# Kernel optimization log

Hardware: AMD Instinct MI355X
Metric: run time of the kernel (lower is better)

The kernel has to match this reference:

```python
import jax, jax.numpy as jnp
import numpy as np

B_SCALE = 1.3195079565048218
N_LEVELS = 16
BASE_RES = 16
MAX_PARAMS = 2 ** 19
N_POINTS = 1048576
PRIMES = (1, 2654435761, 805459861)  # uint32 hash primes (Instant-NGP)


def _level_meta():
    offsets, sizes, inds = [], [], []
    off = 0
    for i in range(N_LEVELS):
        res = int(np.ceil(BASE_RES * np.exp(i * np.log(B_SCALE)) - 1.0)) + 1
        p = res ** 3
        if p % 8 != 0:
            p = ((p + 7) // 8) * 8
        p = min(MAX_PARAMS, p)
        offsets.append(off)
        sizes.append(p)
        inds.append(res ** 3 <= p)  # dense (under_hash) vs hashed level
        off += p
    return offsets, sizes, inds, off


OFFSETS, SIZES, INDICATORS, TOTAL_PARAMS = _level_meta()
TOTAL_HASH_SIZE = TOTAL_PARAMS * 2  # == 11445040


def _encode_level(x01, table2, level):
    # x01: [N,3] in [0,1]; table2: [total_params, 2]
    scale = np.float32(BASE_RES * np.exp(level * np.log(B_SCALE)) - 1.0)
    resolution = np.uint32(np.ceil(scale) + 1)
    map_size = np.uint32(SIZES[level])
    pos = x01 * scale + 0.5
    grid_f = jnp.floor(pos)
    frac = pos - grid_f                           # [N,3] trilinear weights
    grid = grid_f.astype(jnp.uint32)              # [N,3]
    feat = jnp.zeros((x01.shape[0], 2), dtype=table2.dtype)
    primes = np.array(PRIMES, dtype=np.uint32)
    stride = np.array([1, int(resolution), int(resolution) * int(resolution)], dtype=np.uint32)
    for idx in range(8):  # 8 grid corners
        sel = np.array([(idx >> d) & 1 for d in range(3)], dtype=np.uint32)
        corner = grid + sel                       # [N,3] uint32
        w = jnp.prod(jnp.where(sel[None, :] == 1, frac, 1.0 - frac), axis=-1)  # [N]
        if INDICATORS[level]:
            c = corner * stride[None, :]
            h = c[:, 0] + c[:, 1] + c[:, 2]       # under_hash (dense indexing)
        else:
            c = corner * primes[None, :]          # uint32 wraparound multiply
            h = c[:, 0] ^ c[:, 1] ^ c[:, 2]       # fast_hash
        index = (h % map_size).astype(jnp.int32) + np.int32(OFFSETS[level])
        feat = feat + w[:, None] * table2[index]  # gather + trilinear blend
    return feat


def setup_inputs() -> dict:
    key = jax.random.key(0)
    k1, k2 = jax.random.split(key)
    positions = jax.random.uniform(k1, (N_POINTS, 3), dtype=jnp.float32, minval=-1.0, maxval=1.0)
    # random_initialize: (rand*2-1)*1e-4
    hash_table = jax.random.uniform(k2, (TOTAL_HASH_SIZE,), dtype=jnp.float32, minval=-1e-4, maxval=1e-4)
    return {"positions": positions, "hash_table": hash_table}


def reference(positions, hash_table):
    x01 = (positions + 1.0) * 0.5  # bound = 1
    table2 = hash_table.reshape(-1, 2)
    feats = [_encode_level(x01, table2, l) for l in range(N_LEVELS)]
    return jnp.concatenate(feats, axis=-1)  # [N, 32]
```

## Files before the change

kernel.cpp:

```cpp
#include <hip/hip_runtime.h>
#include <math.h>
#include <stdint.h>

#define NLV 16
#define NDENSE 6
#define NHASH 10

typedef float evf2 __attribute__((ext_vector_type(2)));

struct Params {
  float scale[NLV];
  uint32_t res[NLV];
  uint32_t msize[NLV];
  uint32_t offset[NLV];
};

struct ParamsD {
  float scale[NDENSE];
  uint32_t res[NDENSE];
  uint32_t msize[NDENSE];
  uint32_t offset[NDENSE];
};

__device__ __forceinline__ float ntload(const float* p) {
  return __builtin_nontemporal_load(p);
}

__global__ __launch_bounds__(256) void hash_level_kernel(
    const float* __restrict__ positions,
    const float* __restrict__ tbl,
    float2* __restrict__ tmp,
    float scale, uint32_t mask, int n)
{
  int t = blockIdx.x * 256 + threadIdx.x;
  int p0 = t * 2;
  if (p0 >= n) return;

  float xx[2], yy[2], zz[2];
  {
    evf2 a = __builtin_nontemporal_load(reinterpret_cast<const evf2*>(positions + 3*p0));
    evf2 b = __builtin_nontemporal_load(reinterpret_cast<const evf2*>(positions + 3*p0 + 2));
    evf2 c = __builtin_nontemporal_load(reinterpret_cast<const evf2*>(positions + 3*p0 + 4));
    xx[0] = a.x; yy[0] = a.y; zz[0] = b.x;
    xx[1] = b.y; yy[1] = c.x; zz[1] = c.y;
  }

  float r0[2], r1[2];
  #pragma unroll
  for (int q = 0; q < 2; ++q) {
    float x = (xx[q] + 1.0f) * 0.5f;
    float y = (yy[q] + 1.0f) * 0.5f;
    float z = (zz[q] + 1.0f) * 0.5f;

    float px = x * scale + 0.5f;
    float py = y * scale + 0.5f;
    float pz = z * scale + 0.5f;
    float fx = floorf(px), fy = floorf(py), fz = floorf(pz);
    float tx = px - fx, ty = py - fy, tz = pz - fz;
    uint32_t gx = (uint32_t)fx, gy = (uint32_t)fy, gz = (uint32_t)fz;

    float wxa = 1.0f - tx, wxb = tx;
    float wy_[2] = {1.0f - ty, ty};
    float wz_[2] = {1.0f - tz, tz};

    float f0 = 0.0f, f1 = 0.0f;

    if ((gx & 1u) == 0u) {
      #pragma unroll
      for (int cyz = 0; cyz < 4; ++cyz) {
        uint32_t cy = gy + (cyz & 1u);
        uint32_t cz = gz + (cyz >> 1);
        uint32_t hy = (cy * 2654435761u) ^ (cz * 805459861u);
        uint32_t ha = (gx ^ hy) & mask;
        float wyz = wy_[cyz & 1u] * wz_[cyz >> 1];
        float wa = wxa * wyz, wb = wxb * wyz;
        const float4 t4 = *reinterpret_cast<const float4*>(tbl + 2u * (ha & ~1u));
        float2 ta, tb;
        if (ha & 1u) { ta.x = t4.z; ta.y = t4.w; tb.x = t4.x; tb.y = t4.y; }
        else         { ta.x = t4.x; ta.y = t4.y; tb.x = t4.z; tb.y = t4.w; }
        f0 += wa * ta.x; f1 += wa * ta.y;
        f0 += wb * tb.x; f1 += wb * tb.y;
      }
    } else {
      #pragma unroll
      for (int cyz = 0; cyz < 4; ++cyz) {
        uint32_t cy = gy + (cyz & 1u);
        uint32_t cz = gz + (cyz >> 1);
        uint32_t hy = (cy * 2654435761u) ^ (cz * 805459861u);
        uint32_t ha = (gx ^ hy) & mask;
        uint32_t hb = ((gx + 1u) ^ hy) & mask;
        float wyz = wy_[cyz & 1u] * wz_[cyz >> 1];
        float wa = wxa * wyz, wb = wxb * wyz;
        const float2 ta = *reinterpret_cast<const float2*>(tbl + 2u * ha);
        const float2 tb = *reinterpret_cast<const float2*>(tbl + 2u * hb);
        f0 += wa * ta.x; f1 += wa * ta.y;
        f0 += wb * tb.x; f1 += wb * tb.y;
      }
    }
    r0[q] = f0; r1[q] = f1;
  }

  evf2 v0; v0.x = r0[0]; v0.y = r1[0];
  __builtin_nontemporal_store(v0, reinterpret_cast<evf2*>(tmp + p0));
  if (p0 + 1 < n) {
    evf2 v1; v1.x = r0[1]; v1.y = r1[1];
    __builtin_nontemporal_store(v1, reinterpret_cast<evf2*>(tmp + p0 + 1));
  }
}

__global__ __launch_bounds__(256) void dense_kernel(
    const float* __restrict__ positions,
    const float* __restrict__ table,
    float2* __restrict__ tmp,
    ParamsD prm, int n)
{
  int p = blockIdx.x * 256 + threadIdx.x;
  if (p >= n) return;

  float x = (ntload(positions + 3*p+0) + 1.0f) * 0.5f;
  float y = (ntload(positions + 3*p+1) + 1.0f) * 0.5f;
  float z = (ntload(positions + 3*p+2) + 1.0f) * 0.5f;

  #pragma unroll
  for (int l = 0; l < NDENSE; ++l) {
    const float s = prm.scale[l];
    const uint32_t res = prm.res[l];
    const uint32_t ms = prm.msize[l];
    const float* __restrict__ tbl = table + 2u * prm.offset[l];
    const uint32_t res2 = res * res;

    float px = x * s + 0.5f;
    float py = y * s + 0.5f;
    float pz = z * s + 0.5f;
    float fx = floorf(px), fy = floorf(py), fz = floorf(pz);
    float tx = px - fx, ty = py - fy, tz = pz - fz;
    uint32_t gx = (uint32_t)fx, gy = (uint32_t)fy, gz = (uint32_t)fz;

    float wxa = 1.0f - tx, wxb = tx;
    float wy_[2] = {1.0f - ty, ty};
    float wz_[2] = {1.0f - tz, tz};

    float f0 = 0.0f, f1 = 0.0f;
    #pragma unroll
    for (int cyz = 0; cyz < 4; ++cyz) {
      uint32_t cy = gy + (cyz & 1u);
      uint32_t cz = gz + ((cyz >> 1) & 1u);
      uint32_t h = gx + cy * res + cz * res2;
      if (h >= ms) h -= ms;
      float wyz = wy_[cyz & 1u] * wz_[(cyz >> 1) & 1u];
      float2 ta, tb;
      if (h + 1u < ms) {
        const float4 t4 = *reinterpret_cast<const float4*>(tbl + 2u * h);
        ta.x = t4.x; ta.y = t4.y; tb.x = t4.z; tb.y = t4.w;
      } else {
        ta = *reinterpret_cast<const float2*>(tbl + 2u * h);
        tb = *reinterpret_cast<const float2*>(tbl);
      }
      float wa = wxa * wyz, wb = wxb * wyz;
      f0 += wa * ta.x; f1 += wa * ta.y;
      f0 += wb * tb.x; f1 += wb * tb.y;
    }
    evf2 v; v.x = f0; v.y = f1;
    __builtin_nontemporal_store(v,
        reinterpret_cast<evf2*>(tmp + (size_t)(NHASH + l) * n + p));
  }
}

__global__ __launch_bounds__(256) void stream_pack_kernel(
    const float2* __restrict__ tmp,
    float* __restrict__ out, int n)
{
  int p = blockIdx.x * 256 + threadIdx.x;
  if (p >= n) return;

  evf2 dv[NDENSE];
  #pragma unroll
  for (int j = 0; j < NDENSE; ++j)
    dv[j] = __builtin_nontemporal_load(
        reinterpret_cast<const evf2*>(tmp + (size_t)(NHASH + j) * n + p));
  evf2 hv[NHASH];
  #pragma unroll
  for (int j = 0; j < NHASH; ++j)
    hv[j] = __builtin_nontemporal_load(
        reinterpret_cast<const evf2*>(tmp + (size_t)j * n + p));

  float4* o = reinterpret_cast<float4*>(out + (size_t)p * 32u);
  #pragma unroll
  for (int j = 0; j < 3; ++j)
    o[j] = make_float4(dv[2*j].x, dv[2*j].y, dv[2*j+1].x, dv[2*j+1].y);
  #pragma unroll
  for (int j = 0; j < 5; ++j)
    o[3 + j] = make_float4(hv[2*j].x, hv[2*j].y, hv[2*j+1].x, hv[2*j+1].y);
}

__global__ __launch_bounds__(256) void dense_pack_kernel(
    const float* __restrict__ positions,
    const float* __restrict__ table,
    const float2* __restrict__ tmp,
    float* __restrict__ out,
    ParamsD prm, int n)
{
  int p = blockIdx.x * 256 + threadIdx.x;
  if (p >= n) return;

  float x = (ntload(positions + 3*p+0) + 1.0f) * 0.5f;
  float y = (ntload(positions + 3*p+1) + 1.0f) * 0.5f;
  float z = (ntload(positions + 3*p+2) + 1.0f) * 0.5f;

  float acc[2*NDENSE];

  #pragma unroll
  for (int l = 0; l < NDENSE; ++l) {
    const float s = prm.scale[l];
    const uint32_t res = prm.res[l];
    const uint32_t ms = prm.msize[l];
    const float* __restrict__ tbl = table + 2u * prm.offset[l];
    const uint32_t res2 = res * res;

    float px = x * s + 0.5f;
    float py = y * s + 0.5f;
    float pz = z * s + 0.5f;
    float fx = floorf(px), fy = floorf(py), fz = floorf(pz);
    float tx = px - fx, ty = py - fy, tz = pz - fz;
    uint32_t gx = (uint32_t)fx, gy = (uint32_t)fy, gz = (uint32_t)fz;

    float wxa = 1.0f - tx, wxb = tx;
    float wy_[2] = {1.0f - ty, ty};
    float wz_[2] = {1.0f - tz, tz};

    float f0 = 0.0f, f1 = 0.0f;
    #pragma unroll
    for (int cyz = 0; cyz < 4; ++cyz) {
      uint32_t cy = gy + (cyz & 1u);
      uint32_t cz = gz + ((cyz >> 1) & 1u);
      uint32_t h = gx + cy * res + cz * res2;
      if (h >= ms) h -= ms;
      float wyz = wy_[cyz & 1u] * wz_[(cyz >> 1) & 1u];
      float2 ta, tb;
      if (h + 1u < ms) {
        const float4 t4 = *reinterpret_cast<const float4*>(tbl + 2u * h);
        ta.x = t4.x; ta.y = t4.y; tb.x = t4.z; tb.y = t4.w;
      } else {
        ta = *reinterpret_cast<const float2*>(tbl + 2u * h);
        tb = *reinterpret_cast<const float2*>(tbl);
      }
      float wa = wxa * wyz, wb = wxb * wyz;
      f0 += wa * ta.x; f1 += wa * ta.y;
      f0 += wb * tb.x; f1 += wb * tb.y;
    }
    acc[2*l]   = f0;
    acc[2*l+1] = f1;
  }

  evf2 hv[NHASH];
  #pragma unroll
  for (int j = 0; j < NHASH; ++j)
    hv[j] = __builtin_nontemporal_load(
        reinterpret_cast<const evf2*>(tmp + (size_t)j * n + p));

  float4* o = reinterpret_cast<float4*>(out + (size_t)p * 32u);
  o[0] = make_float4(acc[0], acc[1], acc[2],  acc[3]);
  o[1] = make_float4(acc[4], acc[5], acc[6],  acc[7]);
  o[2] = make_float4(acc[8], acc[9], acc[10], acc[11]);
  #pragma unroll
  for (int j = 0; j < 5; ++j)
    o[3 + j] = make_float4(hv[2*j].x, hv[2*j].y, hv[2*j+1].x, hv[2*j+1].y);
}

__global__ __launch_bounds__(256) void hash_enc_kernel(
    const float* __restrict__ positions,
    const float* __restrict__ table,
    float* __restrict__ out,
    Params prm, int n)
{
  int p = blockIdx.x * 256 + threadIdx.x;
  if (p >= n) return;

  float x = (positions[3*p+0] + 1.0f) * 0.5f;
  float y = (positions[3*p+1] + 1.0f) * 0.5f;
  float z = (positions[3*p+2] + 1.0f) * 0.5f;

  float acc[32];

  #pragma unroll
  for (int l = 0; l < NLV; ++l) {
    const float s = prm.scale[l];
    const uint32_t res = prm.res[l];
    const uint32_t ms = prm.msize[l];
    const uint32_t off = prm.offset[l];

    float px = x * s + 0.5f;
    float py = y * s + 0.5f;
    float pz = z * s + 0.5f;
    float fx = floorf(px), fy = floorf(py), fz = floorf(pz);
    float tx = px - fx, ty = py - fy, tz = pz - fz;
    uint32_t gx = (uint32_t)fx, gy = (uint32_t)fy, gz = (uint32_t)fz;

    float wx[2] = {1.0f - tx, tx};
    float wy[2] = {1.0f - ty, ty};
    float wz[2] = {1.0f - tz, tz};

    float f0 = 0.0f, f1 = 0.0f;
    #pragma unroll
    for (int c = 0; c < 8; ++c) {
      uint32_t cx = gx + (c & 1u);
      uint32_t cy = gy + ((c >> 1) & 1u);
      uint32_t cz = gz + ((c >> 2) & 1u);
      uint32_t h;
      if (l < NDENSE) {
        h = cx + cy * res + cz * res * res;
        if (h >= ms) h -= ms;
      } else {
        h = cx ^ (cy * 2654435761u) ^ (cz * 805459861u);
        h &= (ms - 1u);
      }
      float w = (wx[c & 1u] * wy[(c >> 1) & 1u]) * wz[(c >> 2) & 1u];
      const float2 t = *reinterpret_cast<const float2*>(table + 2u * (h + off));
      f0 += w * t.x;
      f1 += w * t.y;
    }
    acc[2*l]   = f0;
    acc[2*l+1] = f1;
  }

  float4* o = reinterpret_cast<float4*>(out + (size_t)p * 32u);
  #pragma unroll
  for (int k = 0; k < 8; ++k)
    o[k] = make_float4(acc[4*k+0], acc[4*k+1], acc[4*k+2], acc[4*k+3]);
}

extern "C" void kernel_launch(void* const* d_in, const int* in_sizes, int n_in,
                              void* d_out, int out_size, void* d_ws, size_t ws_size,
                              hipStream_t stream) {
  const float* positions = (const float*)d_in[0];
  const float* table     = (const float*)d_in[1];
  float* out             = (float*)d_out;
  int n = in_sizes[0] / 3;

  Params prm;
  const double lnb = log(1.3195079565048218);
  uint32_t off = 0;
  for (int l = 0; l < NLV; ++l) {
    double sd = 16.0 * exp((double)l * lnb) - 1.0;
    uint32_t res_meta = (uint32_t)ceil(sd) + 1u;
    uint64_t p3 = (uint64_t)res_meta * res_meta * res_meta;
    uint64_t ps = (p3 % 8ull) ? ((p3 + 7ull) / 8ull) * 8ull : p3;
    if (ps > (1ull << 19)) ps = 1ull << 19;
    float sf = (float)sd;
    uint32_t res_enc = (uint32_t)(ceilf(sf) + 1.0f);
    prm.scale[l]  = sf;
    prm.res[l]    = res_enc;
    prm.msize[l]  = (uint32_t)ps;
    prm.offset[l] = off;
    off += (uint32_t)ps;
  }
  ParamsD pd;
  for (int l = 0; l < NDENSE; ++l) {
    pd.scale[l] = prm.scale[l]; pd.res[l] = prm.res[l];
    pd.msize[l] = prm.msize[l]; pd.offset[l] = prm.offset[l];
  }

  dim3 block(256);
  dim3 gfull((n + 255) / 256);
  dim3 ghash((n/2 + 255) / 256);
  size_t ws16 = (size_t)NLV * (size_t)n * sizeof(float2);
  size_t ws10 = (size_t)NHASH * (size_t)n * sizeof(float2);

  if (ws_size >= ws16) {
    float2* tmp = (float2*)d_ws;
    for (int l = NDENSE; l < NLV; ++l) {
      hipLaunchKernelGGL(hash_level_kernel, ghash, block, 0, stream,
                         positions, table + 2u * prm.offset[l],
                         tmp + (size_t)(l - NDENSE) * n,
                         prm.scale[l], prm.msize[l] - 1u, n);
    }
    hipLaunchKernelGGL(dense_kernel, gfull, block, 0, stream,
                       positions, table, tmp, pd, n);
    hipLaunchKernelGGL(stream_pack_kernel, gfull, block, 0, stream,
                       tmp, out, n);
  } else if (ws_size >= ws10) {
    float2* tmp = (float2*)d_ws;
    for (int l = NDENSE; l < NLV; ++l) {
      hipLaunchKernelGGL(hash_level_kernel, ghash, block, 0, stream,
                         positions, table + 2u * prm.offset[l],
                         tmp + (size_t)(l - NDENSE) * n,
                         prm.scale[l], prm.msize[l] - 1u, n);
    }
    hipLaunchKernelGGL(dense_pack_kernel, gfull, block, 0, stream,
                       positions, table, tmp, out, pd, n);
  } else {
    hipLaunchKernelGGL(hash_enc_kernel, gfull, block, 0, stream,
                       positions, table, out, prm, n);
  }
}
```

Baseline: 485.1 us.

## Spatially bin-sort points before encoding to improve gather locality

Adds a counting sort of points into a 32^3 spatial grid (histogram, single-block scan, atomic scatter) so that neighbouring points are processed together in the per-level hash and dense kernels. The intent is better cache locality for the table gathers. Results are then scattered back to their original order through an LDS-staged pack kernel. This adds several extra passes, atomics and an indirect output write, and the bin order inside each cell is nondeterministic. It also removes the 10-level workspace fallback path.

```diff
diff --git a/kernel.cpp b/kernel.cpp
--- a/kernel.cpp
+++ b/kernel.cpp
@@ -5,6 +5,8 @@
 #define NLV 16
 #define NDENSE 6
 #define NHASH 10
+#define SORT_RES 32
+#define NBINS (SORT_RES * SORT_RES * SORT_RES)
 
 typedef float evf2 __attribute__((ext_vector_type(2)));
 
@@ -24,6 +26,67 @@
 
 __device__ __forceinline__ float ntload(const float* p) {
   return __builtin_nontemporal_load(p);
+}
+
+__device__ __forceinline__ uint32_t cell_key(float xr, float yr, float zr) {
+  float x01 = (xr + 1.0f) * 0.5f;
+  float y01 = (yr + 1.0f) * 0.5f;
+  float z01 = (zr + 1.0f) * 0.5f;
+  int cx = (int)(x01 * (float)SORT_RES);
+  int cy = (int)(y01 * (float)SORT_RES);
+  int cz = (int)(z01 * (float)SORT_RES);
+  cx = cx < 0 ? 0 : (cx > SORT_RES-1 ? SORT_RES-1 : cx);
+  cy = cy < 0 ? 0 : (cy > SORT_RES-1 ? SORT_RES-1 : cy);
+  cz = cz < 0 ? 0 : (cz > SORT_RES-1 ? SORT_RES-1 : cz);
+  return (uint32_t)(cx | (cy << 5) | (cz << 10));
+}
+
+__global__ __launch_bounds__(256) void zero_bins_kernel(uint32_t* bins) {
+  int i = blockIdx.x * 256 + threadIdx.x;
+  if (i < NBINS) bins[i] = 0u;
+}
+
+__global__ __launch_bounds__(256) void hist_kernel(
+    const float* __restrict__ positions, uint32_t* __restrict__ bins, int n) {
+  int p = blockIdx.x * 256 + threadIdx.x;
+  if (p >= n) return;
+  float x = positions[3*p], y = positions[3*p+1], z = positions[3*p+2];
+  atomicAdd(&bins[cell_key(x, y, z)], 1u);
+}
+
+__global__ __launch_bounds__(1024) void scan_kernel(
+    const uint32_t* __restrict__ bins, uint32_t* __restrict__ cursor) {
+  __shared__ uint32_t lds[1024];
+  int t = threadIdx.x;
+  uint32_t local[32];
+  uint32_t s = 0;
+  #pragma unroll
+  for (int j = 0; j < 32; ++j) { local[j] = bins[t*32 + j]; s += local[j]; }
+  lds[t] = s;
+  __syncthreads();
+  for (int off = 1; off < 1024; off <<= 1) {
+    uint32_t v = (t >= off) ? lds[t - off] : 0u;
+    __syncthreads();
+    lds[t] += v;
+    __syncthreads();
+  }
+  uint32_t run = lds[t] - s;
+  #pragma unroll
+  for (int j = 0; j < 32; ++j) { cursor[t*32 + j] = run; run += local[j]; }
+}
+
+__global__ __launch_bounds__(256) void scatter_kernel(
+    const float* __restrict__ positions, uint32_t* __restrict__ cursor,
+    float* __restrict__ sortedPos, uint32_t* __restrict__ origIdx, int n) {
+  int p = blockIdx.x * 256 + threadIdx.x;
+  if (p >= n) return;
+  float x = positions[3*p], y = positions[3*p+1], z = positions[3*p+2];
+  uint32_t k = cell_key(x, y, z);
+  uint32_t dst = atomicAdd(&cursor[k], 1u);
+  sortedPos[3*dst]   = x;
+  sortedPos[3*dst+1] = y;
+  sortedPos[3*dst+2] = z;
+  origIdx[dst] = p;
 }
 
 __global__ __launch_bounds__(256) void hash_level_kernel(
@@ -166,9 +229,56 @@
   }
 }
 
+__global__ __launch_bounds__(256) void pack_scatter_kernel(
+    const float2* __restrict__ tmp,
+    const uint32_t* __restrict__ origIdx,
+    float* __restrict__ out, int n)
+{
+  __shared__ float lds[256 * 33];
+  int t = threadIdx.x;
+  int base = blockIdx.x * 256;
+  int p = base + t;
+
+  if (p < n) {
+    #pragma unroll
+    for (int j = 0; j < NDENSE; ++j) {
+      evf2 v = __builtin_nontemporal_load(
+          reinterpret_cast<const evf2*>(tmp + (size_t)(NHASH + j) * n + p));
+      lds[t*33 + 2*j]     = v.x;
+      lds[t*33 + 2*j + 1] = v.y;
+    }
+    #pragma unroll
+    for (int j = 0; j < NHASH; ++j) {
+      evf2 v = __builtin_nontemporal_load(
+          reinterpret_cast<const evf2*>(tmp + (size_t)j * n + p));
+      lds[t*33 + 12 + 2*j]     = v.x;
+      lds[t*33 + 12 + 2*j + 1] = v.y;
+    }
+  }
+  __syncthreads();
+
+  if (base + 256 <= n) {
+    int qr = t >> 3, r = t & 7;
+    #pragma unroll
+    for (int k = 0; k < 8; ++k) {
+      int q = k * 32 + qr;
+      uint32_t oi = origIdx[base + q];
+      float4 v = make_float4(lds[q*33 + r*4], lds[q*33 + r*4 + 1],
+                             lds[q*33 + r*4 + 2], lds[q*33 + r*4 + 3]);
+      reinterpret_cast<float4*>(out + (size_t)oi * 32u)[r] = v;
+    }
+  } else if (p < n) {
+    uint32_t oi = origIdx[p];
+    float4* o = reinterpret_cast<float4*>(out + (size_t)oi * 32u);
+    #pragma unroll
+    for (int k = 0; k < 8; ++k)
+      o[k] = make_float4(lds[t*33 + 4*k], lds[t*33 + 4*k + 1],
+                         lds[t*33 + 4*k + 2], lds[t*33 + 4*k + 3]);
+  }
+}
+
 __global__ __launch_bounds__(256) void stream_pack_kernel(
-    const float2* __restrict__ tmp,
-    float* __restrict__ out, int n)
+    const float2* __restrict__ tmp, float* __restrict__ out, int n)
 {
   int p = blockIdx.x * 256 + threadIdx.x;
   if (p >= n) return;
@@ -188,80 +298,6 @@
   #pragma unroll
   for (int j = 0; j < 3; ++j)
     o[j] = make_float4(dv[2*j].x, dv[2*j].y, dv[2*j+1].x, dv[2*j+1].y);
-  #pragma unroll
-  for (int j = 0; j < 5; ++j)
-    o[3 + j] = make_float4(hv[2*j].x, hv[2*j].y, hv[2*j+1].x, hv[2*j+1].y);
-}
-
-__global__ __launch_bounds__(256) void dense_pack_kernel(
-    const float* __restrict__ positions,
-    const float* __restrict__ table,
-    const float2* __restrict__ tmp,
-    float* __restrict__ out,
-    ParamsD prm, int n)
-{
-  int p = blockIdx.x * 256 + threadIdx.x;
-  if (p >= n) return;
-
-  float x = (ntload(positions + 3*p+0) + 1.0f) * 0.5f;
-  float y = (ntload(positions + 3*p+1) + 1.0f) * 0.5f;
-  float z = (ntload(positions + 3*p+2) + 1.0f) * 0.5f;
-
-  float acc[2*NDENSE];
-
-  #pragma unroll
-  for (int l = 0; l < NDENSE; ++l) {
-    const float s = prm.scale[l];
-    const uint32_t res = prm.res[l];
-    const uint32_t ms = prm.msize[l];
-    const float* __restrict__ tbl = table + 2u * prm.offset[l];
-    const uint32_t res2 = res * res;
-
-    float px = x * s + 0.5f;
-    float py = y * s + 0.5f;
-    float pz = z * s + 0.5f;
-    float fx = floorf(px), fy = floorf(py), fz = floorf(pz);
-    float tx = px - fx, ty = py - fy, tz = pz - fz;
-    uint32_t gx = (uint32_t)fx, gy = (uint32_t)fy, gz = (uint32_t)fz;
-
-    float wxa = 1.0f - tx, wxb = tx;
-    float wy_[2] = {1.0f - ty, ty};
-    float wz_[2] = {1.0f - tz, tz};
-
-    float f0 = 0.0f, f1 = 0.0f;
-    #pragma unroll
-    for (int cyz = 0; cyz < 4; ++cyz) {
-      uint32_t cy = gy + (cyz & 1u);
-      uint32_t cz = gz + ((cyz >> 1) & 1u);
-      uint32_t h = gx + cy * res + cz * res2;
-      if (h >= ms) h -= ms;
-      float wyz = wy_[cyz & 1u] * wz_[(cyz >> 1) & 1u];
-      float2 ta, tb;
-      if (h + 1u < ms) {
-        const float4 t4 = *reinterpret_cast<const float4*>(tbl + 2u * h);
-        ta.x = t4.x; ta.y = t4.y; tb.x = t4.z; tb.y = t4.w;
-      } else {
-        ta = *reinterpret_cast<const float2*>(tbl + 2u * h);
-        tb = *reinterpret_cast<const float2*>(tbl);
-      }
-      float wa = wxa * wyz, wb = wxb * wyz;
-      f0 += wa * ta.x; f1 += wa * ta.y;
-      f0 += wb * tb.x; f1 += wb * tb.y;
-    }
-    acc[2*l]   = f0;
-    acc[2*l+1] = f1;
-  }
-
-  evf2 hv[NHASH];
-  #pragma unroll
-  for (int j = 0; j < NHASH; ++j)
-    hv[j] = __builtin_nontemporal_load(
-        reinterpret_cast<const evf2*>(tmp + (size_t)j * n + p));
-
-  float4* o = reinterpret_cast<float4*>(out + (size_t)p * 32u);
-  o[0] = make_float4(acc[0], acc[1], acc[2],  acc[3]);
-  o[1] = make_float4(acc[4], acc[5], acc[6],  acc[7]);
-  o[2] = make_float4(acc[8], acc[9], acc[10], acc[11]);
   #pragma unroll
   for (int j = 0; j < 5; ++j)
     o[3 + j] = make_float4(hv[2*j].x, hv[2*j].y, hv[2*j+1].x, hv[2*j+1].y);
@@ -363,10 +399,41 @@
   dim3 block(256);
   dim3 gfull((n + 255) / 256);
   dim3 ghash((n/2 + 255) / 256);
-  size_t ws16 = (size_t)NLV * (size_t)n * sizeof(float2);
-  size_t ws10 = (size_t)NHASH * (size_t)n * sizeof(float2);
-
-  if (ws_size >= ws16) {
+
+  size_t tmp_b  = (size_t)NLV * n * sizeof(float2);
+  size_t sp_off = tmp_b;
+  size_t oi_off = sp_off + (size_t)3 * n * sizeof(float);
+  size_t bn_off = oi_off + (size_t)n * sizeof(uint32_t);
+  size_t cu_off = bn_off + (size_t)NBINS * sizeof(uint32_t);
+  size_t total  = cu_off + (size_t)NBINS * sizeof(uint32_t);
+  size_t ws16   = tmp_b;
+
+  char* wsb = (char*)d_ws;
+
+  if (ws_size >= total && (n % 2) == 0) {
+    float2*   tmp       = (float2*)wsb;
+    float*    sortedPos = (float*)(wsb + sp_off);
+    uint32_t* origIdx   = (uint32_t*)(wsb + oi_off);
+    uint32_t* bins      = (uint32_t*)(wsb + bn_off);
+    uint32_t* cursor    = (uint32_t*)(wsb + cu_off);
+
+    hipLaunchKernelGGL(zero_bins_kernel, dim3((NBINS + 255) / 256), block, 0, stream, bins);
+    hipLaunchKernelGGL(hist_kernel, gfull, block, 0, stream, positions, bins, n);
+    hipLaunchKernelGGL(scan_kernel, dim3(1), dim3(1024), 0, stream, bins, cursor);
+    hipLaunchKernelGGL(scatter_kernel, gfull, block, 0, stream,
+                       positions, cursor, sortedPos, origIdx, n);
+
+    for (int l = NDENSE; l < NLV; ++l) {
+      hipLaunchKernelGGL(hash_level_kernel, ghash, block, 0, stream,
+                         sortedPos, table + 2u * prm.offset[l],
+                         tmp + (size_t)(l - NDENSE) * n,
+                         prm.scale[l], prm.msize[l] - 1u, n);
+    }
+    hipLaunchKernelGGL(dense_kernel, gfull, block, 0, stream,
+                       sortedPos, table, tmp, pd, n);
+    hipLaunchKernelGGL(pack_scatter_kernel, gfull, block, 0, stream,
+                       tmp, origIdx, out, n);
+  } else if (ws_size >= ws16 && (n % 2) == 0) {
     float2* tmp = (float2*)d_ws;
     for (int l = NDENSE; l < NLV; ++l) {
       hipLaunchKernelGGL(hash_level_kernel, ghash, block, 0, stream,
@@ -378,16 +445,6 @@
                        positions, table, tmp, pd, n);
     hipLaunchKernelGGL(stream_pack_kernel, gfull, block, 0, stream,
                        tmp, out, n);
-  } else if (ws_size >= ws10) {
-    float2* tmp = (float2*)d_ws;
-    for (int l = NDENSE; l < NLV; ++l) {
-      hipLaunchKernelGGL(hash_level_kernel, ghash, block, 0, stream,
-                         positions, table + 2u * prm.offset[l],
-                         tmp + (size_t)(l - NDENSE) * n,
-                         prm.scale[l], prm.msize[l] - 1u, n);
-    }
-    hipLaunchKernelGGL(dense_pack_kernel, gfull, block, 0, stream,
-                       positions, table, tmp, out, pd, n);
   } else {
     hipLaunchKernelGGL(hash_enc_kernel, gfull, block, 0, stream,
                        positions, table, out, prm, n);
```

Measured after the change: 448.7 us. -7.5%, faster.
